# Kernel tuning notes

Hardware: AMD Instinct MI355X
Metric: run time of the kernel (lower is better)

## Reference

```python
import jax, jax.numpy as jnp
import numpy as np

B, H, W = 16, 720, 1280


def setup_inputs() -> dict:
    key = jax.random.key(0)
    k1, k2, k3, k4 = jax.random.split(key, 4)
    real_B = jax.random.normal(k1, (B, 1, H, W), jnp.float32)
    offset = jax.random.normal(k2, (B, 2, H, W), jnp.float32)  # (dy, dx) per pixel
    weight = jax.random.normal(k3, (1, 1, 1, 1), jnp.float32)  # DCNv2 1x1 kernel
    bias = jax.random.normal(k4, (1,), jnp.float32)
    return {"real_B": real_B, "offset": offset, "weight": weight, "bias": bias}


def _bilinear_sample(img, py, px):
    """img: [B,H,W]; py,px: [B,H,W] float sample coords. Zero padding outside."""
    Bb, Hh, Ww = img.shape
    y0 = jnp.floor(py)
    x0 = jnp.floor(px)
    y1, x1 = y0 + 1.0, x0 + 1.0
    wy1 = py - y0
    wy0 = 1.0 - wy1
    wx1 = px - x0
    wx0 = 1.0 - wx1
    flat = img.reshape(Bb, Hh * Ww)

    def gather(yi, xi):
        valid = (yi >= 0) & (yi <= Hh - 1) & (xi >= 0) & (xi <= Ww - 1)
        yc = jnp.clip(yi, 0, Hh - 1).astype(jnp.int32)
        xc = jnp.clip(xi, 0, Ww - 1).astype(jnp.int32)
        idx = (yc * Ww + xc).reshape(Bb, -1)
        v = jnp.take_along_axis(flat, idx, axis=1).reshape(Bb, Hh, Ww)
        return jnp.where(valid, v, 0.0)

    return (wy0 * wx0 * gather(y0, x0) + wy0 * wx1 * gather(y0, x1)
            + wy1 * wx0 * gather(y1, x0) + wy1 * wx1 * gather(y1, x1))


def reference(real_B, offset, weight, bias):
    # chunk into 2 along channel then cat -> identity for C=2, kept for fidelity
    o1, o2 = jnp.split(offset, 2, axis=1)
    offset = jnp.concatenate((o1, o2), axis=1)
    Bb, _, Hh, Ww = offset.shape
    mask = jnp.ones((Bb, 1, Hh, Ww), offset.dtype)
    # DCNv2 offset layout for k=1: channel 0 = dy, channel 1 = dx
    off_y, off_x = offset[:, 0], offset[:, 1]
    gy, gx = jnp.meshgrid(jnp.arange(Hh, dtype=offset.dtype),
                          jnp.arange(Ww, dtype=offset.dtype), indexing="ij")
    py = gy[None] + off_y  # [B,H,W]
    px = gx[None] + off_x
    sampled = _bilinear_sample(real_B[:, 0], py, px)  # [B,H,W]
    out = weight[0, 0, 0, 0] * sampled * mask[:, 0] + bias[0]
    return out[:, None]  # [B,1,H,W]
```

## Files before the change

### kernel.cpp

```cpp
#include <hip/hip_runtime.h>


#define NB 16
#define IH 720
#define IW 1280
#define TW 128
#define TH 16
#define HALO_Y 6
#define HX_L 8
#define SROWS (TH + 2*HALO_Y + 1)
#define SCOLS 148
#define SLOTQ (SCOLS/4)
#define SLOTS (SROWS * SLOTQ)

__global__ __launch_bounds__(256) void blurnet_tile(
    const float* __restrict__ img,
    const float* __restrict__ offset,
    const float* __restrict__ weight,
    const float* __restrict__ bias,
    float* __restrict__ out)
{
    __shared__ float ls[SROWS][SCOLS];

    const int HW = IH * IW;
    const int tilesX = IW / TW;
    const int tilesY = IH / TH;
    const int nwg = NB * tilesX * tilesY;

    int bid = blockIdx.x;
    int tile = (bid & 7) * (nwg >> 3) + (bid >> 3);

    int b  = tile / (tilesX * tilesY);
    int tr = tile % (tilesX * tilesY);
    int ty0 = (tr / tilesX) * TH;
    int tx0 = (tr % tilesX) * TW;

    const float* imgb = img + b * HW;

    for (int s = threadIdx.x; s < SLOTS; s += 256) {
        int r  = s / SLOTQ;
        int c4 = s % SLOTQ;
        int gr = ty0 - HALO_Y + r;
        int gc = tx0 - HX_L + c4 * 4;
        float4 v;
        if (gr >= 0 && gr < IH && gc >= 0 && gc + 3 < IW) {
            v = *reinterpret_cast<const float4*>(imgb + gr * IW + gc);
        } else {
            float t0 = 0.f, t1 = 0.f, t2 = 0.f, t3 = 0.f;
            if (gr >= 0 && gr < IH) {
                if (gc     >= 0 && gc     < IW) t0 = imgb[gr * IW + gc];
                if (gc + 1 >= 0 && gc + 1 < IW) t1 = imgb[gr * IW + gc + 1];
                if (gc + 2 >= 0 && gc + 2 < IW) t2 = imgb[gr * IW + gc + 2];
                if (gc + 3 >= 0 && gc + 3 < IW) t3 = imgb[gr * IW + gc + 3];
            }
            v = make_float4(t0, t1, t2, t3);
        }
        *reinterpret_cast<float4*>(&ls[r][c4 * 4]) = v;
    }
    __syncthreads();

    const float w   = weight[0];
    const float bsv = bias[0];
    const float* offy = offset + (size_t)b * 2 * HW;
    const float* offx = offy + HW;

    #pragma unroll
    for (int qq = 0; qq < 2; ++qq) {
        int q   = threadIdx.x + qq * 256;
        int row = q >> 5;
        int col = (q & 31) << 2;
        int gy  = ty0 + row;
        int gx0 = tx0 + col;
        int base = gy * IW + gx0;

        float4 oy = *reinterpret_cast<const float4*>(offy + base);
        float4 ox = *reinterpret_cast<const float4*>(offx + base);
        float oys[4] = {oy.x, oy.y, oy.z, oy.w};
        float oxs[4] = {ox.x, ox.y, ox.z, ox.w};
        float res[4];

        #pragma unroll
        for (int k = 0; k < 4; ++k) {
            float py = (float)gy + oys[k];
            float px = (float)(gx0 + k) + oxs[k];
            float fy0 = floorf(py);
            float fx0 = floorf(px);
            int y0 = (int)fy0;
            int x0 = (int)fx0;
            float wy1 = py - fy0, wy0 = 1.0f - wy1;
            float wx1 = px - fx0, wx0 = 1.0f - wx1;

            int lr = y0 - (ty0 - HALO_Y);
            int lc = x0 - (tx0 - HX_L);
            float v00, v01, v10, v11;
            if (lr >= 0 && lr + 1 < SROWS && lc >= 0 && lc + 1 < SCOLS) {
                v00 = ls[lr][lc];
                v01 = ls[lr][lc + 1];
                v10 = ls[lr + 1][lc];
                v11 = ls[lr + 1][lc + 1];
            } else {
                bool yv0 = (y0 >= 0)     && (y0 < IH);
                bool yv1 = (y0 + 1 >= 0) && (y0 + 1 < IH);
                bool xv0 = (x0 >= 0)     && (x0 < IW);
                bool xv1 = (x0 + 1 >= 0) && (x0 + 1 < IW);
                v00 = (yv0 && xv0) ? imgb[y0 * IW + x0]           : 0.0f;
                v01 = (yv0 && xv1) ? imgb[y0 * IW + x0 + 1]       : 0.0f;
                v10 = (yv1 && xv0) ? imgb[(y0 + 1) * IW + x0]     : 0.0f;
                v11 = (yv1 && xv1) ? imgb[(y0 + 1) * IW + x0 + 1] : 0.0f;
            }
            float s = wy0 * (wx0 * v00 + wx1 * v01) + wy1 * (wx0 * v10 + wx1 * v11);
            res[k] = w * s + bsv;
        }
        *reinterpret_cast<float4*>(out + (size_t)b * HW + base) =
            make_float4(res[0], res[1], res[2], res[3]);
    }
}

extern "C" void kernel_launch(void* const* d_in, const int* in_sizes, int n_in,
                              void* d_out, int out_size, void* d_ws, size_t ws_size,
                              hipStream_t stream) {
    const float* img = (const float*)d_in[0];
    const float* off = (const float*)d_in[1];
    const float* wt  = (const float*)d_in[2];
    const float* bs  = (const float*)d_in[3];
    float* out = (float*)d_out;

    const int blocks = NB * (IH / TH) * (IW / TW);
    blurnet_tile<<<blocks, 256, 0, stream>>>(img, off, wt, bs, out);
}
```

Before: 235.6 us.

## Prefetch offsets before the barrier and remap threads to one column per thread

```diff
diff --git a/kernel.cpp b/kernel.cpp
--- a/kernel.cpp
+++ b/kernel.cpp
@@ -57,62 +57,58 @@
         }
         *reinterpret_cast<float4*>(&ls[r][c4 * 4]) = v;
     }
+
+    const float* offy = offset + (size_t)b * 2 * HW;
+    const float* offx = offy + HW;
+    int r0  = threadIdx.x >> 7;
+    int col = threadIdx.x & 127;
+    int gx  = tx0 + col;
+    int base0 = (ty0 + r0) * IW + gx;
+
+    float oys[8], oxs[8];
+    #pragma unroll
+    for (int i = 0; i < 8; ++i) oys[i] = offy[base0 + i * 2 * IW];
+    #pragma unroll
+    for (int i = 0; i < 8; ++i) oxs[i] = offx[base0 + i * 2 * IW];
+
     __syncthreads();
 
     const float w   = weight[0];
     const float bsv = bias[0];
-    const float* offy = offset + (size_t)b * 2 * HW;
-    const float* offx = offy + HW;
+    const float fgx = (float)gx;
 
     #pragma unroll
-    for (int qq = 0; qq < 2; ++qq) {
-        int q   = threadIdx.x + qq * 256;
-        int row = q >> 5;
-        int col = (q & 31) << 2;
-        int gy  = ty0 + row;
-        int gx0 = tx0 + col;
-        int base = gy * IW + gx0;
+    for (int i = 0; i < 8; ++i) {
+        int gy = ty0 + r0 + 2 * i;
+        float py = (float)gy + oys[i];
+        float px = fgx + oxs[i];
+        float fy0 = floorf(py);
+        float fx0 = floorf(px);
+        int y0 = (int)fy0;
+        int x0 = (int)fx0;
+        float wy1 = py - fy0, wy0 = 1.0f - wy1;
+        float wx1 = px - fx0, wx0 = 1.0f - wx1;
 
-        float4 oy = *reinterpret_cast<const float4*>(offy + base);
-        float4 ox = *reinterpret_cast<const float4*>(offx + base);
-        float oys[4] = {oy.x, oy.y, oy.z, oy.w};
-        float oxs[4] = {ox.x, ox.y, ox.z, ox.w};
-        float res[4];
-
-        #pragma unroll
-        for (int k = 0; k < 4; ++k) {
-            float py = (float)gy + oys[k];
-            float px = (float)(gx0 + k) + oxs[k];
-            float fy0 = floorf(py);
-            float fx0 = floorf(px);
-            int y0 = (int)fy0;
-            int x0 = (int)fx0;
-            float wy1 = py - fy0, wy0 = 1.0f - wy1;
-            float wx1 = px - fx0, wx0 = 1.0f - wx1;
-
-            int lr = y0 - (ty0 - HALO_Y);
-            int lc = x0 - (tx0 - HX_L);
-            float v00, v01, v10, v11;
-            if (lr >= 0 && lr + 1 < SROWS && lc >= 0 && lc + 1 < SCOLS) {
-                v00 = ls[lr][lc];
-                v01 = ls[lr][lc + 1];
-                v10 = ls[lr + 1][lc];
-                v11 = ls[lr + 1][lc + 1];
-            } else {
-                bool yv0 = (y0 >= 0)     && (y0 < IH);
-                bool yv1 = (y0 + 1 >= 0) && (y0 + 1 < IH);
-                bool xv0 = (x0 >= 0)     && (x0 < IW);
-                bool xv1 = (x0 + 1 >= 0) && (x0 + 1 < IW);
-                v00 = (yv0 && xv0) ? imgb[y0 * IW + x0]           : 0.0f;
-                v01 = (yv0 && xv1) ? imgb[y0 * IW + x0 + 1]       : 0.0f;
-                v10 = (yv1 && xv0) ? imgb[(y0 + 1) * IW + x0]     : 0.0f;
-                v11 = (yv1 && xv1) ? imgb[(y0 + 1) * IW + x0 + 1] : 0.0f;
-            }
-            float s = wy0 * (wx0 * v00 + wx1 * v01) + wy1 * (wx0 * v10 + wx1 * v11);
-            res[k] = w * s + bsv;
+        int lr = y0 - (ty0 - HALO_Y);
+        int lc = x0 - (tx0 - HX_L);
+        float v00, v01, v10, v11;
+        if (lr >= 0 && lr + 1 < SROWS && lc >= 0 && lc + 1 < SCOLS) {
+            v00 = ls[lr][lc];
+            v01 = ls[lr][lc + 1];
+            v10 = ls[lr + 1][lc];
+            v11 = ls[lr + 1][lc + 1];
+        } else {
+            bool yv0 = (y0 >= 0)     && (y0 < IH);
+            bool yv1 = (y0 + 1 >= 0) && (y0 + 1 < IH);
+            bool xv0 = (x0 >= 0)     && (x0 < IW);
+            bool xv1 = (x0 + 1 >= 0) && (x0 + 1 < IW);
+            v00 = (yv0 && xv0) ? imgb[y0 * IW + x0]           : 0.0f;
+            v01 = (yv0 && xv1) ? imgb[y0 * IW + x0 + 1]       : 0.0f;
+            v10 = (yv1 && xv0) ? imgb[(y0 + 1) * IW + x0]     : 0.0f;
+            v11 = (yv1 && xv1) ? imgb[(y0 + 1) * IW + x0 + 1] : 0.0f;
         }
-        *reinterpret_cast<float4*>(out + (size_t)b * HW + base) =
-            make_float4(res[0], res[1], res[2], res[3]);
+        float s = wy0 * (wx0 * v00 + wx1 * v01) + wy1 * (wx0 * v10 + wx1 * v11);
+        out[(size_t)b * HW + base0 + i * 2 * IW] = w * s + bsv;
     }
 }
 
```

New measurement: 236.7 us. No clear change (+0.5%).
